# Performance work log

Measured on AMD Instinct MI355X. Metric: run time of the kernel, lower is better.

Reference implementation:

```python
import jax, jax.numpy as jnp
import numpy as np

NUM_HEADS = 8
DIM_HEAD = 64
EMBED_DIM = NUM_HEADS * DIM_HEAD  # 512


def setup_inputs() -> dict:
    key = jax.random.key(0)
    k1, k2, k3, k4, k5 = jax.random.split(key, 5)
    B, D, S, L = 1, EMBED_DIM, 256, 256
    x = jax.random.normal(k1, (B, D, S, L), dtype=jnp.float32)
    # 1x1 conv weights as [out_ch, in_ch] matrices; small init keeps softmax logits sane
    Wr = jax.random.normal(k2, (3 * D, D), dtype=jnp.float32) * 0.02
    br = jax.random.normal(k3, (3 * D,), dtype=jnp.float32) * 0.02
    Wc = jax.random.normal(k4, (3 * D, D), dtype=jnp.float32) * 0.02
    bc = jax.random.normal(k5, (3 * D,), dtype=jnp.float32) * 0.02
    return {"x": x, "Wr": Wr, "br": br, "Wc": Wc, "bc": bc}


def _qkv(x, W, b):
    # 1x1 Conv2d == per-pixel matmul over channels
    B, D, S, L = x.shape
    proj = jnp.einsum('oc,bcsl->bosl', W, x) + b[None, :, None, None]
    q, k, v = jnp.split(proj, 3, axis=1)
    shp = (B, NUM_HEADS, DIM_HEAD, S, L)
    return q.reshape(shp), k.reshape(shp), v.reshape(shp)


def reference(x, Wr, br, Wc, bc):
    B, D, S, L = x.shape
    # --- row attention (attend along L within each row s) ---
    q, k, v = _qkv(x, Wr, br)
    row_attn = jnp.einsum('bhcsi,bhcsj->bhsij', q, k)          # [B,H,S,L,L]
    row_attn = jax.nn.softmax(row_attn, axis=-1)
    row_out = jnp.einsum('bhsij,bhdsj->bhdsi', row_attn, v)    # [B,H,dh,S,L]
    out = x + row_out.reshape(B, D, S, L)
    # --- column attention (attend along S within each column l) ---
    q, k, v = _qkv(out, Wc, bc)
    col_attn = jnp.einsum('bhcil,bhcjl->bhijl', q, k)          # [B,H,S,S,L]
    col_attn = jax.nn.softmax(col_attn, axis=-2)               # softmax over j (dim=-2)
    col_out = jnp.einsum('bhijl,bhdjl->bhdil', col_attn, v)    # [B,H,dh,S,L]
    out = out + col_out.reshape(B, D, S, L)
    return out
```

## Files before the change

kernel.cpp:

```cpp
#include <hip/hip_runtime.h>

typedef __bf16 bf16_t;
typedef __attribute__((ext_vector_type(8))) __bf16 bf16x8;
typedef __attribute__((ext_vector_type(4))) float f32x4;
typedef __attribute__((ext_vector_type(16))) float f32x16;

#define NH   8
#define DH   64
#define DD   512
#define NPIX 65536

__device__ __forceinline__ unsigned short f2bf(float f) {
  unsigned int u = __builtin_bit_cast(unsigned int, f);
  u += 0x7fffu + ((u >> 16) & 1u);
  return (unsigned short)(u >> 16);
}
__device__ __forceinline__ float bf2f(unsigned short b) {
  return __builtin_bit_cast(float, ((unsigned int)b) << 16);
}
__device__ __forceinline__ unsigned cvtpk(float a, float b) {
  unsigned r;
  asm("v_cvt_pk_bf16_f32 %0, %1, %2" : "=v"(r) : "v"(a), "v"(b));
  return r;
}

__device__ __forceinline__ void gload_lds16(const void* g, void* l) {
  __builtin_amdgcn_global_load_lds(
      (const __attribute__((address_space(1))) void*)(uintptr_t)g,
      (__attribute__((address_space(3))) void*)(uintptr_t)l, 16, 0, 0);
}

__global__ __launch_bounds__(256) void k_cvt(const float* __restrict__ in,
                                             unsigned short* __restrict__ out, int n4) {
  int i = blockIdx.x * 256 + threadIdx.x;
  if (i >= n4) return;
  float4 v = ((const float4*)in)[i];
  ushort4 o; o.x = f2bf(v.x); o.y = f2bf(v.y); o.z = f2bf(v.z); o.w = f2bf(v.w);
  ((ushort4*)out)[i] = o;
}

__global__ __launch_bounds__(256) void k_cvt_transpose(const float* __restrict__ x,
                                                       unsigned short* __restrict__ xt) {
  __shared__ unsigned short Xs[64 * 68];
  int p0 = blockIdx.x * 64, c0 = blockIdx.y * 64;
  int t = threadIdx.x;
  for (int rep = 0; rep < 4; ++rep) {
    int f = rep * 256 + t, i = f >> 4, jj = f & 15;
    float4 v = *(const float4*)(x + (size_t)(c0 + i) * NPIX + p0 + jj * 4);
    ushort4 o; o.x = f2bf(v.x); o.y = f2bf(v.y); o.z = f2bf(v.z); o.w = f2bf(v.w);
    *(ushort4*)(Xs + i * 68 + jj * 4) = o;
  }
  __syncthreads();
  int j = t >> 2, q = t & 3;
  unsigned short* dst = xt + (size_t)(p0 + j) * DD + c0 + q * 16;
  for (int h2 = 0; h2 < 2; ++h2) {
    union { unsigned short u[8]; uint4 v; } pk;
    for (int cc = 0; cc < 8; ++cc) pk.u[cc] = Xs[(q * 16 + h2 * 8 + cc) * 68 + j];
    *(uint4*)(dst + h2 * 8) = pk.v;
  }
}

template <int IS_COL>
__global__ __launch_bounds__(512, 2) void k_fused(const unsigned short* __restrict__ panel,
                                                  const unsigned short* __restrict__ Wb,
                                                  const float* __restrict__ bias,
                                                  const float* __restrict__ x,
                                                  unsigned short* __restrict__ outnat,
                                                  unsigned short* __restrict__ outbt) {
  __shared__ unsigned short smem[57344];
  const int tid = threadIdx.x, lane = tid & 63, wave = tid >> 6;
  const int l31 = lane & 31, hi = lane >> 5;
  int bid = blockIdx.y * 8 + blockIdx.x;
  int lid = (bid & 7) * 256 + (bid >> 3);
  const int h = lid & 7, fix = lid >> 3;
  const size_t pixbase = (size_t)fix * 256;
  const int wm = wave >> 2, wn = wave & 3;
  const int i0w = wave * 32;

  const unsigned short* Pbase = panel + pixbase * 512;

  auto STAGE = [&](int b, int kt) {
    unsigned short* Ab = smem + b * 28672;
    unsigned short* Bb = Ab + 12288;
#pragma unroll
    for (int it = 0; it < 3; ++it) {
      int f = it * 512 + tid;
      int row = f >> 3;
      int cc = (f & 7) ^ (row & 7);
      int grow = (row >> 6) * 512 + h * 64 + (row & 63);
      gload_lds16(Wb + (size_t)grow * 512 + kt * 64 + cc * 8, Ab + f * 8);
    }
#pragma unroll
    for (int it = 0; it < 4; ++it) {
      int f = it * 512 + tid;
      int row = f >> 3;
      int cc = (f & 7) ^ (row & 7);
      gload_lds16(Pbase + (size_t)row * 512 + kt * 64 + cc * 8, Bb + f * 8);
    }
  };

  f32x16 acc[3][2] = {};
  STAGE(0, 0);
  asm volatile("s_waitcnt vmcnt(0)" ::: "memory");
  __syncthreads();
  int cur = 0;
  for (int kt = 0; kt < 8; ++kt) {
    if (kt < 7) STAGE(cur ^ 1, kt + 1);
    const char* Ad = (const char*)smem + cur * 57344;
    const char* Bd = Ad + 24576;
#pragma unroll
    for (int ks = 0; ks < 4; ++ks) {
      bf16x8 afr[3], bfr[2];
#pragma unroll
      for (int mt = 0; mt < 3; ++mt) {
        int r = wm * 96 + mt * 32 + l31;
        afr[mt] = *(const bf16x8*)(Ad + r * 128 + ((ks * 32 + hi * 16) ^ ((r & 7) << 4)));
      }
#pragma unroll
      for (int nt = 0; nt < 2; ++nt) {
        int r = wn * 64 + nt * 32 + l31;
        bfr[nt] = *(const bf16x8*)(Bd + r * 128 + ((ks * 32 + hi * 16) ^ ((r & 7) << 4)));
      }
      __builtin_amdgcn_s_setprio(1);
#pragma unroll
      for (int mt = 0; mt < 3; ++mt)
#pragma unroll
        for (int nt = 0; nt < 2; ++nt)
          acc[mt][nt] = __builtin_amdgcn_mfma_f32_32x32x16_bf16(afr[mt], bfr[nt], acc[mt][nt], 0, 0, 0);
      __builtin_amdgcn_s_setprio(0);
    }
    asm volatile("s_waitcnt vmcnt(0)" ::: "memory");
    __syncthreads();
    cur ^= 1;
  }
  unsigned short* Qt = smem;
  unsigned short* Kt = smem + 16384;
  unsigned short* Vn = smem + 32768;
#pragma unroll
  for (int mt = 0; mt < 3; ++mt) {
    int rb = wm * 96 + mt * 32 + 4 * hi;
#pragma unroll
    for (int q = 0; q < 4; ++q) {
      int crow = rb + 8 * q;
      int sel = crow >> 6, r64 = crow & 63;
      f32x4 bv = *(const f32x4*)(bias + sel * 512 + h * 64 + r64);
#pragma unroll
      for (int nt = 0; nt < 2; ++nt) {
        int col = wn * 64 + nt * 32 + l31;
        float v0 = acc[mt][nt][q * 4 + 0] + bv.x;
        float v1 = acc[mt][nt][q * 4 + 1] + bv.y;
        float v2 = acc[mt][nt][q * 4 + 2] + bv.z;
        float v3 = acc[mt][nt][q * 4 + 3] + bv.w;
        if (sel < 2) {
          ushort4 pk;
          pk.x = f2bf(v0); pk.y = f2bf(v1); pk.z = f2bf(v2); pk.w = f2bf(v3);
          char* base = (char*)(sel ? Kt : Qt);
          *(ushort4*)(base + col * 128 + ((r64 * 2) ^ ((col & 7) << 4))) = pk;
        } else {
          char* base = (char*)Vn;
          *(unsigned short*)(base + (r64 + 0) * 512 + ((col * 2) ^ (((r64 + 0) & 7) << 4))) = f2bf(v0);
          *(unsigned short*)(base + (r64 + 1) * 512 + ((col * 2) ^ (((r64 + 1) & 7) << 4))) = f2bf(v1);
          *(unsigned short*)(base + (r64 + 2) * 512 + ((col * 2) ^ (((r64 + 2) & 7) << 4))) = f2bf(v2);
          *(unsigned short*)(base + (r64 + 3) * 512 + ((col * 2) ^ (((r64 + 3) & 7) << 4))) = f2bf(v3);
        }
      }
    }
  }
  __syncthreads();

  const int swz = (l31 & 7) << 4;
  bf16x8 qf[4];
  {
    const char* qrow = (const char*)Qt + (i0w + l31) * 128;
#pragma unroll
    for (int ks = 0; ks < 4; ++ks)
      qf[ks] = *(const bf16x8*)(qrow + ((ks * 32 + hi * 16) ^ swz));
  }

  f32x16 s[8] = {};
  __builtin_amdgcn_s_setprio(1);
#pragma unroll
  for (int jt = 0; jt < 8; ++jt) {
    const char* kr = (const char*)Kt + (jt * 32 + l31) * 128;
#pragma unroll
    for (int ks = 0; ks < 4; ++ks) {
      bf16x8 kf = *(const bf16x8*)(kr + ((ks * 32 + hi * 16) ^ swz));
      s[jt] = __builtin_amdgcn_mfma_f32_32x32x16_bf16(kf, qf[ks], s[jt], 0, 0, 0);
    }
  }
  __builtin_amdgcn_s_setprio(0);

  float mx = -3.4e38f;
#pragma unroll
  for (int jt = 0; jt < 8; ++jt)
#pragma unroll
    for (int r = 0; r < 16; ++r) mx = fmaxf(mx, s[jt][r]);
  mx = fmaxf(mx, __shfl_xor(mx, 32, 64));
  float sum = 0.f;
#pragma unroll
  for (int jt = 0; jt < 8; ++jt)
#pragma unroll
    for (int r = 0; r < 16; ++r) {
      float p = __expf(s[jt][r] - mx);
      s[jt][r] = p; sum += p;
    }
  sum += __shfl_xor(sum, 32, 64);
  float inv = 1.f / sum;

  bf16x8 pf[16];
#pragma unroll
  for (int jt = 0; jt < 8; ++jt)
#pragma unroll
    for (int kb = 0; kb < 2; ++kb) {
      int kt2 = jt * 2 + kb;
      unsigned pA0 = cvtpk(s[jt][kb * 8 + 0] * inv, s[jt][kb * 8 + 1] * inv);
      unsigned pA1 = cvtpk(s[jt][kb * 8 + 2] * inv, s[jt][kb * 8 + 3] * inv);
      unsigned pB0 = cvtpk(s[jt][kb * 8 + 4] * inv, s[jt][kb * 8 + 5] * inv);
      unsigned pB1 = cvtpk(s[jt][kb * 8 + 6] * inv, s[jt][kb * 8 + 7] * inv);
      unsigned s0 = hi ? pA0 : pB0;
      unsigned s1 = hi ? pA1 : pB1;
      unsigned r0 = (unsigned)__shfl_xor((int)s0, 32, 64);
      unsigned r1 = (unsigned)__shfl_xor((int)s1, 32, 64);
      union { unsigned u[4]; bf16x8 v; } pk_;
      pk_.u[0] = hi ? r0 : pA0;
      pk_.u[1] = hi ? r1 : pA1;
      pk_.u[2] = hi ? pB0 : r0;
      pk_.u[3] = hi ? pB1 : r1;
      pf[kt2] = pk_.v;
    }

  f32x16 o[2] = {};
  __builtin_amdgcn_s_setprio(1);
#pragma unroll
  for (int dt = 0; dt < 2; ++dt) {
    const char* vr = (const char*)Vn + (dt * 32 + l31) * 512;
#pragma unroll
    for (int kt2 = 0; kt2 < 16; ++kt2) {
      bf16x8 vf = *(const bf16x8*)(vr + ((kt2 * 32 + hi * 16) ^ swz));
      o[dt] = __builtin_amdgcn_mfma_f32_32x32x16_bf16(pf[kt2], vf, o[dt], 0, 0, 0);
    }
  }
  __builtin_amdgcn_s_setprio(0);

  if (!IS_COL) {
#pragma unroll
    for (int dt = 0; dt < 2; ++dt) {
      int c = h * 64 + dt * 32 + l31;
      const float* xb = x + (size_t)c * NPIX + pixbase + i0w;
      unsigned short* ob = outnat + (size_t)c * NPIX + pixbase + i0w;
#pragma unroll
      for (int q = 0; q < 4; ++q) {
        int ib = q * 8 + hi * 4;
        float4 xv = *(const float4*)(xb + ib);
        float4 vv;
        vv.x = o[dt][q * 4 + 0] + xv.x;
        vv.y = o[dt][q * 4 + 1] + xv.y;
        vv.z = o[dt][q * 4 + 2] + xv.z;
        vv.w = o[dt][q * 4 + 3] + xv.w;
        ushort4 pk;
        pk.x = f2bf(vv.x); pk.y = f2bf(vv.y); pk.z = f2bf(vv.z); pk.w = f2bf(vv.w);
        *(ushort4*)(ob + ib) = pk;
        o[dt][q * 4 + 0] = vv.x; o[dt][q * 4 + 1] = vv.y;
        o[dt][q * 4 + 2] = vv.z; o[dt][q * 4 + 3] = vv.w;
      }
    }
    __syncthreads();
    unsigned short* Obt = smem;
#pragma unroll
    for (int dt = 0; dt < 2; ++dt) {
      int d = dt * 32 + l31;
#pragma unroll
      for (int q = 0; q < 4; ++q)
#pragma unroll
        for (int m = 0; m < 4; ++m)
          Obt[(i0w + q * 8 + hi * 4 + m) * 72 + d] = f2bf(o[dt][q * 4 + m]);
    }
    __syncthreads();
    int row = tid >> 1, half = tid & 1;
    const unsigned short* src = Obt + row * 72 + half * 32;
    unsigned short* dst = outbt + ((size_t)row * 256 + fix) * 512 + h * 64 + half * 32;
#pragma unroll
    for (int c4 = 0; c4 < 4; ++c4)
      *(uint4*)(dst + c4 * 8) = *(const uint4*)(src + c4 * 8);
  } else {
#pragma unroll
    for (int dt = 0; dt < 2; ++dt) {
      int c = h * 64 + dt * 32 + l31;
      unsigned short* ob = outnat + (size_t)c * NPIX + pixbase + i0w;
#pragma unroll
      for (int q = 0; q < 4; ++q) {
        ushort4 pkv;
        pkv.x = f2bf(o[dt][q * 4 + 0]);
        pkv.y = f2bf(o[dt][q * 4 + 1]);
        pkv.z = f2bf(o[dt][q * 4 + 2]);
        pkv.w = f2bf(o[dt][q * 4 + 3]);
        *(ushort4*)(ob + q * 8 + hi * 4) = pkv;
      }
    }
  }
}

__global__ __launch_bounds__(256) void k_final(const unsigned short* __restrict__ colt,
                                               const unsigned short* __restrict__ out1nat,
                                               float* __restrict__ out) {
  __shared__ unsigned short Xs[64 * 68];
  int c = blockIdx.y;
  int lt = blockIdx.x & 3, st = blockIdx.x >> 2;
  int l0 = lt * 64, s0 = st * 64;
  int t = threadIdx.x;
  for (int rep = 0; rep < 4; ++rep) {
    int f = rep * 256 + t, li = f >> 4, jj = f & 15;
    ushort4 v = *(const ushort4*)(colt + (size_t)c * NPIX + (size_t)(l0 + li) * 256 + s0 + jj * 4);
    *(ushort4*)(Xs + li * 68 + jj * 4) = v;
  }
  __syncthreads();
  int si = t >> 2, q = t & 3;
  size_t rowoff = (size_t)c * NPIX + (size_t)(s0 + si) * 256 + l0 + q * 16;
  float* drow = out + rowoff;
  for (int h4 = 0; h4 < 4; ++h4) {
    ushort4 nv = *(const ushort4*)(out1nat + rowoff + h4 * 4);
    float4 a;
    a.x = bf2f(nv.x) + bf2f(Xs[(q * 16 + h4 * 4 + 0) * 68 + si]);
    a.y = bf2f(nv.y) + bf2f(Xs[(q * 16 + h4 * 4 + 1) * 68 + si]);
    a.z = bf2f(nv.z) + bf2f(Xs[(q * 16 + h4 * 4 + 2) * 68 + si]);
    a.w = bf2f(nv.w) + bf2f(Xs[(q * 16 + h4 * 4 + 3) * 68 + si]);
    *(float4*)(drow + h4 * 4) = a;
  }
}

extern "C" void kernel_launch(void* const* d_in, const int* in_sizes, int n_in,
                              void* d_out, int out_size, void* d_ws, size_t ws_size,
                              hipStream_t stream) {
  const float* x  = (const float*)d_in[0];
  const float* Wr = (const float*)d_in[1];
  const float* br = (const float*)d_in[2];
  const float* Wc = (const float*)d_in[3];
  const float* bc = (const float*)d_in[4];
  float* out = (float*)d_out;
  char* ws = (char*)d_ws;
  unsigned short* xT     = (unsigned short*)(ws);
  unsigned short* o1bt   = (unsigned short*)(ws + 67108864);
  unsigned short* colout = (unsigned short*)(ws + 134217728);
  unsigned short* o1nat  = (unsigned short*)(ws + 201326592);
  unsigned short* Wrb    = (unsigned short*)(ws + 268435456);
  unsigned short* Wcb    = (unsigned short*)(ws + 270008320);

  k_cvt<<<768, 256, 0, stream>>>(Wr, Wrb, 196608);
  k_cvt<<<768, 256, 0, stream>>>(Wc, Wcb, 196608);
  k_cvt_transpose<<<dim3(1024, 8), 256, 0, stream>>>(x, xT);
  k_fused<0><<<dim3(8, 256), 512, 0, stream>>>(xT, Wrb, br, x, o1nat, o1bt);
  k_fused<1><<<dim3(8, 256), 512, 0, stream>>>(o1bt, Wcb, bc, nullptr, colout, nullptr);
  k_final<<<dim3(16, 512), 256, 0, stream>>>(colout, o1nat, out);
}
```

Baseline: 505.7 us.

## Process two heads per block and prefetch next head's first stage during attention

Each fused block now handles two consecutive heads, halving the grid, and gives Q/K/V their own LDS region so the first projection stage for the second head can be issued while the first head's attention runs. The x residual loads are also hoisted before the attention math. The aim is to hide the GEMM prologue latency and cut block launch overhead. In exchange LDS use per block grows (about 152KB), which may allow only one resident block per CU instead of two, and there are half as many blocks.

Result: slower. 992.8 us (+96.3%).

```diff
diff --git a/kernel.cpp b/kernel.cpp
--- a/kernel.cpp
+++ b/kernel.cpp
@@ -67,19 +67,22 @@
                                                   const float* __restrict__ x,
                                                   unsigned short* __restrict__ outnat,
                                                   unsigned short* __restrict__ outbt) {
-  __shared__ unsigned short smem[57344];
+  __shared__ unsigned short smem[77824];
   const int tid = threadIdx.x, lane = tid & 63, wave = tid >> 6;
   const int l31 = lane & 31, hi = lane >> 5;
   int bid = blockIdx.y * 8 + blockIdx.x;
-  int lid = (bid & 7) * 256 + (bid >> 3);
-  const int h = lid & 7, fix = lid >> 3;
+  int lid = (bid & 7) * 128 + (bid >> 3);
+  const int hp = lid & 3, fix = lid >> 2;
   const size_t pixbase = (size_t)fix * 256;
   const int wm = wave >> 2, wn = wave & 3;
   const int i0w = wave * 32;
 
   const unsigned short* Pbase = panel + pixbase * 512;
-
-  auto STAGE = [&](int b, int kt) {
+  unsigned short* Qt = smem + 28672;
+  unsigned short* Kt = smem + 45056;
+  unsigned short* Vn = smem + 61440;
+
+  auto STAGE = [&](int b, int kt, int hS) {
     unsigned short* Ab = smem + b * 28672;
     unsigned short* Bb = Ab + 12288;
 #pragma unroll
@@ -87,7 +90,7 @@
       int f = it * 512 + tid;
       int row = f >> 3;
       int cc = (f & 7) ^ (row & 7);
-      int grow = (row >> 6) * 512 + h * 64 + (row & 63);
+      int grow = (row >> 6) * 512 + hS * 64 + (row & 63);
       gload_lds16(Wb + (size_t)grow * 512 + kt * 64 + cc * 8, Ab + f * 8);
     }
 #pragma unroll
@@ -99,203 +102,218 @@
     }
   };
 
-  f32x16 acc[3][2] = {};
-  STAGE(0, 0);
-  asm volatile("s_waitcnt vmcnt(0)" ::: "memory");
-  __syncthreads();
-  int cur = 0;
-  for (int kt = 0; kt < 8; ++kt) {
-    if (kt < 7) STAGE(cur ^ 1, kt + 1);
-    const char* Ad = (const char*)smem + cur * 57344;
-    const char* Bd = Ad + 24576;
-#pragma unroll
-    for (int ks = 0; ks < 4; ++ks) {
-      bf16x8 afr[3], bfr[2];
-#pragma unroll
-      for (int mt = 0; mt < 3; ++mt) {
-        int r = wm * 96 + mt * 32 + l31;
-        afr[mt] = *(const bf16x8*)(Ad + r * 128 + ((ks * 32 + hi * 16) ^ ((r & 7) << 4)));
-      }
-#pragma unroll
-      for (int nt = 0; nt < 2; ++nt) {
-        int r = wn * 64 + nt * 32 + l31;
-        bfr[nt] = *(const bf16x8*)(Bd + r * 128 + ((ks * 32 + hi * 16) ^ ((r & 7) << 4)));
-      }
-      __builtin_amdgcn_s_setprio(1);
-#pragma unroll
-      for (int mt = 0; mt < 3; ++mt)
-#pragma unroll
-        for (int nt = 0; nt < 2; ++nt)
-          acc[mt][nt] = __builtin_amdgcn_mfma_f32_32x32x16_bf16(afr[mt], bfr[nt], acc[mt][nt], 0, 0, 0);
-      __builtin_amdgcn_s_setprio(0);
-    }
+  float4 xv[2][4];
+
+  STAGE(0, 0, hp * 2);
+  for (int hh = 0; hh < 2; ++hh) {
+    const int h = hp * 2 + hh;
     asm volatile("s_waitcnt vmcnt(0)" ::: "memory");
     __syncthreads();
-    cur ^= 1;
-  }
-  unsigned short* Qt = smem;
-  unsigned short* Kt = smem + 16384;
-  unsigned short* Vn = smem + 32768;
-#pragma unroll
-  for (int mt = 0; mt < 3; ++mt) {
-    int rb = wm * 96 + mt * 32 + 4 * hi;
-#pragma unroll
-    for (int q = 0; q < 4; ++q) {
-      int crow = rb + 8 * q;
-      int sel = crow >> 6, r64 = crow & 63;
-      f32x4 bv = *(const f32x4*)(bias + sel * 512 + h * 64 + r64);
-#pragma unroll
-      for (int nt = 0; nt < 2; ++nt) {
-        int col = wn * 64 + nt * 32 + l31;
-        float v0 = acc[mt][nt][q * 4 + 0] + bv.x;
-        float v1 = acc[mt][nt][q * 4 + 1] + bv.y;
-        float v2 = acc[mt][nt][q * 4 + 2] + bv.z;
-        float v3 = acc[mt][nt][q * 4 + 3] + bv.w;
-        if (sel < 2) {
+
+    f32x16 acc[3][2] = {};
+    int cur = 0;
+    for (int kt = 0; kt < 8; ++kt) {
+      if (kt < 7) STAGE(cur ^ 1, kt + 1, h);
+      const char* Ad = (const char*)smem + cur * 57344;
+      const char* Bd = Ad + 24576;
+#pragma unroll
+      for (int ks = 0; ks < 4; ++ks) {
+        bf16x8 afr[3], bfr[2];
+#pragma unroll
+        for (int mt = 0; mt < 3; ++mt) {
+          int r = wm * 96 + mt * 32 + l31;
+          afr[mt] = *(const bf16x8*)(Ad + r * 128 + ((ks * 32 + hi * 16) ^ ((r & 7) << 4)));
+        }
+#pragma unroll
+        for (int nt = 0; nt < 2; ++nt) {
+          int r = wn * 64 + nt * 32 + l31;
+          bfr[nt] = *(const bf16x8*)(Bd + r * 128 + ((ks * 32 + hi * 16) ^ ((r & 7) << 4)));
+        }
+        __builtin_amdgcn_s_setprio(1);
+#pragma unroll
+        for (int mt = 0; mt < 3; ++mt)
+#pragma unroll
+          for (int nt = 0; nt < 2; ++nt)
+            acc[mt][nt] = __builtin_amdgcn_mfma_f32_32x32x16_bf16(afr[mt], bfr[nt], acc[mt][nt], 0, 0, 0);
+        __builtin_amdgcn_s_setprio(0);
+      }
+      asm volatile("s_waitcnt vmcnt(0)" ::: "memory");
+      __syncthreads();
+      cur ^= 1;
+    }
+
+    if (hh == 0) STAGE(0, 0, h + 1);
+
+#pragma unroll
+    for (int mt = 0; mt < 3; ++mt) {
+      int rb = wm * 96 + mt * 32 + 4 * hi;
+#pragma unroll
+      for (int q = 0; q < 4; ++q) {
+        int crow = rb + 8 * q;
+        int sel = crow >> 6, r64 = crow & 63;
+        f32x4 bv = *(const f32x4*)(bias + sel * 512 + h * 64 + r64);
+#pragma unroll
+        for (int nt = 0; nt < 2; ++nt) {
+          int col = wn * 64 + nt * 32 + l31;
+          float v0 = acc[mt][nt][q * 4 + 0] + bv.x;
+          float v1 = acc[mt][nt][q * 4 + 1] + bv.y;
+          float v2 = acc[mt][nt][q * 4 + 2] + bv.z;
+          float v3 = acc[mt][nt][q * 4 + 3] + bv.w;
+          if (sel < 2) {
+            ushort4 pk;
+            pk.x = f2bf(v0); pk.y = f2bf(v1); pk.z = f2bf(v2); pk.w = f2bf(v3);
+            char* base = (char*)(sel ? Kt : Qt);
+            *(ushort4*)(base + col * 128 + ((r64 * 2) ^ ((col & 7) << 4))) = pk;
+          } else {
+            char* base = (char*)Vn;
+            *(unsigned short*)(base + (r64 + 0) * 512 + ((col * 2) ^ (((r64 + 0) & 7) << 4))) = f2bf(v0);
+            *(unsigned short*)(base + (r64 + 1) * 512 + ((col * 2) ^ (((r64 + 1) & 7) << 4))) = f2bf(v1);
+            *(unsigned short*)(base + (r64 + 2) * 512 + ((col * 2) ^ (((r64 + 2) & 7) << 4))) = f2bf(v2);
+            *(unsigned short*)(base + (r64 + 3) * 512 + ((col * 2) ^ (((r64 + 3) & 7) << 4))) = f2bf(v3);
+          }
+        }
+      }
+    }
+    if constexpr (!IS_COL) {
+#pragma unroll
+      for (int dt = 0; dt < 2; ++dt) {
+        int c = h * 64 + dt * 32 + l31;
+        const float* xb = x + (size_t)c * NPIX + pixbase + i0w;
+#pragma unroll
+        for (int q = 0; q < 4; ++q)
+          xv[dt][q] = *(const float4*)(xb + q * 8 + hi * 4);
+      }
+    }
+    __syncthreads();
+
+    const int swz = (l31 & 7) << 4;
+    bf16x8 qf[4];
+    {
+      const char* qrow = (const char*)Qt + (i0w + l31) * 128;
+#pragma unroll
+      for (int ks = 0; ks < 4; ++ks)
+        qf[ks] = *(const bf16x8*)(qrow + ((ks * 32 + hi * 16) ^ swz));
+    }
+
+    f32x16 s[8] = {};
+    __builtin_amdgcn_s_setprio(1);
+#pragma unroll
+    for (int jt = 0; jt < 8; ++jt) {
+      const char* kr = (const char*)Kt + (jt * 32 + l31) * 128;
+#pragma unroll
+      for (int ks = 0; ks < 4; ++ks) {
+        bf16x8 kf = *(const bf16x8*)(kr + ((ks * 32 + hi * 16) ^ swz));
+        s[jt] = __builtin_amdgcn_mfma_f32_32x32x16_bf16(kf, qf[ks], s[jt], 0, 0, 0);
+      }
+    }
+    __builtin_amdgcn_s_setprio(0);
+
+    float mx = -3.4e38f;
+#pragma unroll
+    for (int jt = 0; jt < 8; ++jt)
+#pragma unroll
+      for (int r = 0; r < 16; ++r) mx = fmaxf(mx, s[jt][r]);
+    mx = fmaxf(mx, __shfl_xor(mx, 32, 64));
+    float sum = 0.f;
+#pragma unroll
+    for (int jt = 0; jt < 8; ++jt)
+#pragma unroll
+      for (int r = 0; r < 16; ++r) {
+        float p = __expf(s[jt][r] - mx);
+        s[jt][r] = p; sum += p;
+      }
+    sum += __shfl_xor(sum, 32, 64);
+    float inv = 1.f / sum;
+
+    bf16x8 pf[16];
+#pragma unroll
+    for (int jt = 0; jt < 8; ++jt)
+#pragma unroll
+      for (int kb = 0; kb < 2; ++kb) {
+        int kt2 = jt * 2 + kb;
+        unsigned pA0 = cvtpk(s[jt][kb * 8 + 0] * inv, s[jt][kb * 8 + 1] * inv);
+        unsigned pA1 = cvtpk(s[jt][kb * 8 + 2] * inv, s[jt][kb * 8 + 3] * inv);
+        unsigned pB0 = cvtpk(s[jt][kb * 8 + 4] * inv, s[jt][kb * 8 + 5] * inv);
+        unsigned pB1 = cvtpk(s[jt][kb * 8 + 6] * inv, s[jt][kb * 8 + 7] * inv);
+        unsigned s0 = hi ? pA0 : pB0;
+        unsigned s1 = hi ? pA1 : pB1;
+        unsigned r0 = (unsigned)__shfl_xor((int)s0, 32, 64);
+        unsigned r1 = (unsigned)__shfl_xor((int)s1, 32, 64);
+        union { unsigned u[4]; bf16x8 v; } pk_;
+        pk_.u[0] = hi ? r0 : pA0;
+        pk_.u[1] = hi ? r1 : pA1;
+        pk_.u[2] = hi ? pB0 : r0;
+        pk_.u[3] = hi ? pB1 : r1;
+        pf[kt2] = pk_.v;
+      }
+
+    f32x16 o[2] = {};
+    __builtin_amdgcn_s_setprio(1);
+#pragma unroll
+    for (int dt = 0; dt < 2; ++dt) {
+      const char* vr = (const char*)Vn + (dt * 32 + l31) * 512;
+#pragma unroll
+      for (int kt2 = 0; kt2 < 16; ++kt2) {
+        bf16x8 vf = *(const bf16x8*)(vr + ((kt2 * 32 + hi * 16) ^ swz));
+        o[dt] = __builtin_amdgcn_mfma_f32_32x32x16_bf16(pf[kt2], vf, o[dt], 0, 0, 0);
+      }
+    }
+    __builtin_amdgcn_s_setprio(0);
+
+    if constexpr (!IS_COL) {
+#pragma unroll
+      for (int dt = 0; dt < 2; ++dt) {
+        int c = h * 64 + dt * 32 + l31;
+        unsigned short* ob = outnat + (size_t)c * NPIX + pixbase + i0w;
+#pragma unroll
+        for (int q = 0; q < 4; ++q) {
+          int ib = q * 8 + hi * 4;
+          float4 vv;
+          vv.x = o[dt][q * 4 + 0] + xv[dt][q].x;
+          vv.y = o[dt][q * 4 + 1] + xv[dt][q].y;
+          vv.z = o[dt][q * 4 + 2] + xv[dt][q].z;
+          vv.w = o[dt][q * 4 + 3] + xv[dt][q].w;
           ushort4 pk;
-          pk.x = f2bf(v0); pk.y = f2bf(v1); pk.z = f2bf(v2); pk.w = f2bf(v3);
-          char* base = (char*)(sel ? Kt : Qt);
-          *(ushort4*)(base + col * 128 + ((r64 * 2) ^ ((col & 7) << 4))) = pk;
-        } else {
-          char* base = (char*)Vn;
-          *(unsigned short*)(base + (r64 + 0) * 512 + ((col * 2) ^ (((r64 + 0) & 7) << 4))) = f2bf(v0);
-          *(unsigned short*)(base + (r64 + 1) * 512 + ((col * 2) ^ (((r64 + 1) & 7) << 4))) = f2bf(v1);
-          *(unsigned short*)(base + (r64 + 2) * 512 + ((col * 2) ^ (((r64 + 2) & 7) << 4))) = f2bf(v2);
-          *(unsigned short*)(base + (r64 + 3) * 512 + ((col * 2) ^ (((r64 + 3) & 7) << 4))) = f2bf(v3);
-        }
-      }
-    }
-  }
-  __syncthreads();
-
-  const int swz = (l31 & 7) << 4;
-  bf16x8 qf[4];
-  {
-    const char* qrow = (const char*)Qt + (i0w + l31) * 128;
-#pragma unroll
-    for (int ks = 0; ks < 4; ++ks)
-      qf[ks] = *(const bf16x8*)(qrow + ((ks * 32 + hi * 16) ^ swz));
-  }
-
-  f32x16 s[8] = {};
-  __builtin_amdgcn_s_setprio(1);
-#pragma unroll
-  for (int jt = 0; jt < 8; ++jt) {
-    const char* kr = (const char*)Kt + (jt * 32 + l31) * 128;
-#pragma unroll
-    for (int ks = 0; ks < 4; ++ks) {
-      bf16x8 kf = *(const bf16x8*)(kr + ((ks * 32 + hi * 16) ^ swz));
-      s[jt] = __builtin_amdgcn_mfma_f32_32x32x16_bf16(kf, qf[ks], s[jt], 0, 0, 0);
-    }
-  }
-  __builtin_amdgcn_s_setprio(0);
-
-  float mx = -3.4e38f;
-#pragma unroll
-  for (int jt = 0; jt < 8; ++jt)
-#pragma unroll
-    for (int r = 0; r < 16; ++r) mx = fmaxf(mx, s[jt][r]);
-  mx = fmaxf(mx, __shfl_xor(mx, 32, 64));
-  float sum = 0.f;
-#pragma unroll
-  for (int jt = 0; jt < 8; ++jt)
-#pragma unroll
-    for (int r = 0; r < 16; ++r) {
-      float p = __expf(s[jt][r] - mx);
-      s[jt][r] = p; sum += p;
-    }
-  sum += __shfl_xor(sum, 32, 64);
-  float inv = 1.f / sum;
-
-  bf16x8 pf[16];
-#pragma unroll
-  for (int jt = 0; jt < 8; ++jt)
-#pragma unroll
-    for (int kb = 0; kb < 2; ++kb) {
-      int kt2 = jt * 2 + kb;
-      unsigned pA0 = cvtpk(s[jt][kb * 8 + 0] * inv, s[jt][kb * 8 + 1] * inv);
-      unsigned pA1 = cvtpk(s[jt][kb * 8 + 2] * inv, s[jt][kb * 8 + 3] * inv);
-      unsigned pB0 = cvtpk(s[jt][kb * 8 + 4] * inv, s[jt][kb * 8 + 5] * inv);
-      unsigned pB1 = cvtpk(s[jt][kb * 8 + 6] * inv, s[jt][kb * 8 + 7] * inv);
-      unsigned s0 = hi ? pA0 : pB0;
-      unsigned s1 = hi ? pA1 : pB1;
-      unsigned r0 = (unsigned)__shfl_xor((int)s0, 32, 64);
-      unsigned r1 = (unsigned)__shfl_xor((int)s1, 32, 64);
-      union { unsigned u[4]; bf16x8 v; } pk_;
-      pk_.u[0] = hi ? r0 : pA0;
-      pk_.u[1] = hi ? r1 : pA1;
-      pk_.u[2] = hi ? pB0 : r0;
-      pk_.u[3] = hi ? pB1 : r1;
-      pf[kt2] = pk_.v;
-    }
-
-  f32x16 o[2] = {};
-  __builtin_amdgcn_s_setprio(1);
-#pragma unroll
-  for (int dt = 0; dt < 2; ++dt) {
-    const char* vr = (const char*)Vn + (dt * 32 + l31) * 512;
-#pragma unroll
-    for (int kt2 = 0; kt2 < 16; ++kt2) {
-      bf16x8 vf = *(const bf16x8*)(vr + ((kt2 * 32 + hi * 16) ^ swz));
-      o[dt] = __builtin_amdgcn_mfma_f32_32x32x16_bf16(pf[kt2], vf, o[dt], 0, 0, 0);
-    }
-  }
-  __builtin_amdgcn_s_setprio(0);
-
-  if (!IS_COL) {
-#pragma unroll
-    for (int dt = 0; dt < 2; ++dt) {
-      int c = h * 64 + dt * 32 + l31;
-      const float* xb = x + (size_t)c * NPIX + pixbase + i0w;
-      unsigned short* ob = outnat + (size_t)c * NPIX + pixbase + i0w;
-#pragma unroll
-      for (int q = 0; q < 4; ++q) {
-        int ib = q * 8 + hi * 4;
-        float4 xv = *(const float4*)(xb + ib);
-        float4 vv;
-        vv.x = o[dt][q * 4 + 0] + xv.x;
-        vv.y = o[dt][q * 4 + 1] + xv.y;
-        vv.z = o[dt][q * 4 + 2] + xv.z;
-        vv.w = o[dt][q * 4 + 3] + xv.w;
-        ushort4 pk;
-        pk.x = f2bf(vv.x); pk.y = f2bf(vv.y); pk.z = f2bf(vv.z); pk.w = f2bf(vv.w);
-        *(ushort4*)(ob + ib) = pk;
-        o[dt][q * 4 + 0] = vv.x; o[dt][q * 4 + 1] = vv.y;
-        o[dt][q * 4 + 2] = vv.z; o[dt][q * 4 + 3] = vv.w;
-      }
-    }
-    __syncthreads();
-    unsigned short* Obt = smem;
-#pragma unroll
-    for (int dt = 0; dt < 2; ++dt) {
-      int d = dt * 32 + l31;
-#pragma unroll
-      for (int q = 0; q < 4; ++q)
-#pragma unroll
-        for (int m = 0; m < 4; ++m)
-          Obt[(i0w + q * 8 + hi * 4 + m) * 72 + d] = f2bf(o[dt][q * 4 + m]);
-    }
-    __syncthreads();
-    int row = tid >> 1, half = tid & 1;
-    const unsigned short* src = Obt + row * 72 + half * 32;
-    unsigned short* dst = outbt + ((size_t)row * 256 + fix) * 512 + h * 64 + half * 32;
-#pragma unroll
-    for (int c4 = 0; c4 < 4; ++c4)
-      *(uint4*)(dst + c4 * 8) = *(const uint4*)(src + c4 * 8);
-  } else {
-#pragma unroll
-    for (int dt = 0; dt < 2; ++dt) {
-      int c = h * 64 + dt * 32 + l31;
-      unsigned short* ob = outnat + (size_t)c * NPIX + pixbase + i0w;
-#pragma unroll
-      for (int q = 0; q < 4; ++q) {
-        ushort4 pkv;
-        pkv.x = f2bf(o[dt][q * 4 + 0]);
-        pkv.y = f2bf(o[dt][q * 4 + 1]);
-        pkv.z = f2bf(o[dt][q * 4 + 2]);
-        pkv.w = f2bf(o[dt][q * 4 + 3]);
-        *(ushort4*)(ob + q * 8 + hi * 4) = pkv;
-      }
+          pk.x = f2bf(vv.x); pk.y = f2bf(vv.y); pk.z = f2bf(vv.z); pk.w = f2bf(vv.w);
+          *(ushort4*)(ob + ib) = pk;
+          o[dt][q * 4 + 0] = vv.x; o[dt][q * 4 + 1] = vv.y;
+          o[dt][q * 4 + 2] = vv.z; o[dt][q * 4 + 3] = vv.w;
+        }
+      }
+      __syncthreads();
+      unsigned short* Obt = Qt;
+#pragma unroll
+      for (int dt = 0; dt < 2; ++dt) {
+        int d = dt * 32 + l31;
+#pragma unroll
+        for (int q = 0; q < 4; ++q)
+#pragma unroll
+          for (int m = 0; m < 4; ++m)
+            Obt[(i0w + q * 8 + hi * 4 + m) * 72 + d] = f2bf(o[dt][q * 4 + m]);
+      }
+      __syncthreads();
+      int row = tid >> 1, half = tid & 1;
+      const unsigned short* src = Obt + row * 72 + half * 32;
+      unsigned short* dst = outbt + ((size_t)row * 256 + fix) * 512 + h * 64 + half * 32;
+#pragma unroll
+      for (int c4 = 0; c4 < 4; ++c4)
+        *(uint4*)(dst + c4 * 8) = *(const uint4*)(src + c4 * 8);
+    } else {
+#pragma unroll
+      for (int dt = 0; dt < 2; ++dt) {
+        int c = h * 64 + dt * 32 + l31;
+        unsigned short* ob = outnat + (size_t)c * NPIX + pixbase + i0w;
+#pragma unroll
+        for (int q = 0; q < 4; ++q) {
+          ushort4 pkv;
+          pkv.x = f2bf(o[dt][q * 4 + 0]);
+          pkv.y = f2bf(o[dt][q * 4 + 1]);
+          pkv.z = f2bf(o[dt][q * 4 + 2]);
+          pkv.w = f2bf(o[dt][q * 4 + 3]);
+          *(ushort4*)(ob + q * 8 + hi * 4) = pkv;
+        }
+      }
+      __syncthreads();
     }
   }
 }
@@ -348,7 +366,7 @@
   k_cvt<<<768, 256, 0, stream>>>(Wr, Wrb, 196608);
   k_cvt<<<768, 256, 0, stream>>>(Wc, Wcb, 196608);
   k_cvt_transpose<<<dim3(1024, 8), 256, 0, stream>>>(x, xT);
-  k_fused<0><<<dim3(8, 256), 512, 0, stream>>>(xT, Wrb, br, x, o1nat, o1bt);
-  k_fused<1><<<dim3(8, 256), 512, 0, stream>>>(o1bt, Wcb, bc, nullptr, colout, nullptr);
+  k_fused<0><<<dim3(8, 128), 512, 0, stream>>>(xT, Wrb, br, x, o1nat, o1bt);
+  k_fused<1><<<dim3(8, 128), 512, 0, stream>>>(o1bt, Wcb, bc, nullptr, colout, nullptr);
   k_final<<<dim3(16, 512), 256, 0, stream>>>(colout, o1nat, out);
 }
```
